# Kernel tuning notes

Measured on AMD Instinct MI355X. Metric: run time of the kernel, lower is better.

The kernel has to match this reference:

```python
import jax, jax.numpy as jnp
import numpy as np

NAF, NBF, DT = 64, 32, 1
B, GROUP = 2000, 100
P = B * GROUP

def _lin(key, din, dout):
    kw, kb = jax.random.split(key)
    return (jax.random.normal(kw, (din, dout), jnp.float32) * 0.02,
            jax.random.normal(kb, (dout,), jnp.float32) * 0.01)

def setup_inputs() -> dict:
    key = jax.random.key(0)
    ks = jax.random.split(key, 12)
    pairs = jax.random.normal(ks[0], (P, 2 * NAF + NBF), jnp.float32)
    idx_pairs = jnp.full((B,), GROUP, dtype=jnp.int32)
    ref_feats = jax.random.normal(ks[1], (B, 32), jnp.float32)
    aw, ab = _lin(ks[2], NAF, 128)
    bw, bb = _lin(ks[3], NBF, 128)
    p1w, p1b = _lin(ks[4], 384, 512)
    p2w, p2b = _lin(ks[5], 512, 256)
    p3w, p3b = _lin(ks[6], 256, 1024)
    f1w, f1b = _lin(ks[7], 1024, 512)
    f2w, f2b = _lin(ks[8], 512, 32)
    f3w, f3b = _lin(ks[9], 32, DT)
    return dict(pairs=pairs, idx_pairs=idx_pairs, ref_feats=ref_feats,
                aw=aw, ab=ab, bw=bw, bb=bb,
                p1w=p1w, p1b=p1b, p2w=p2w, p2b=p2b, p3w=p3w, p3b=p3b,
                f1w=f1w, f1b=f1b, f2w=f2w, f2b=f2b, f3w=f3w, f3b=f3b)

def reference(pairs, idx_pairs, ref_feats,
              aw, ab, bw, bb,
              p1w, p1b, p2w, p2b, p3w, p3b,
              f1w, f1b, f2w, f2b, f3w, f3b):
    relu = jax.nn.relu
    a1 = relu(pairs[:, :NAF] @ aw + ab)            # [P,128]
    a2 = relu(pairs[:, NAF:2 * NAF] @ aw + ab)     # [P,128]
    be = relu(pairs[:, 2 * NAF:] @ bw + bb)        # [P,128]
    h = jnp.concatenate([a1, a2, be], axis=1)      # [P,384]
    h = relu(h @ p1w + p1b)
    h = relu(h @ p2w + p2b)
    x = h @ p3w + p3b                              # [P,1024]
    nb = idx_pairs.shape[0]
    seg = jnp.repeat(jnp.arange(nb, dtype=jnp.int32), idx_pairs,
                     total_repeat_length=x.shape[0])
    sums = jax.ops.segment_sum(x, seg, num_segments=nb)
    h_pair = sums / idx_pairs[:, None].astype(x.dtype)  # segment mean [B,1024]
    h = relu(h_pair @ f1w + f1b)
    h = relu(h @ f2w + f2b)
    return h @ f3w + f3b                           # [B,1]
```

## Files before the change

kernel.cpp:

```cpp
#include <hip/hip_runtime.h>
#include <cstdint>
#include <cstddef>


typedef __bf16 bf16;
typedef __attribute__((ext_vector_type(8))) __bf16 bf16x8;
typedef __attribute__((ext_vector_type(4))) __bf16 bf16x4;
typedef __attribute__((ext_vector_type(4))) float floatx4;

#define GRP 100
#define NWIN 3125

#define WOFF_AW 0
#define WOFF_BW 8192
#define WOFF_P1 12288
#define WOFF_P2 208896
#define WOFF_P3 339968
#define WOFF_F1 602112
#define WOFF_F2 1126400
#define WOFF_HS 1142784
#define WOFF_HP 4342784
#define WOFF_H2 6390784

#define LSTR_P  168
#define LSTR_H  392
#define LSTR_H2 136
#define LSTR_MS 264

static __device__ __forceinline__ floatx4 mfma16(bf16x8 a, bf16x8 b, floatx4 c) {
  return __builtin_amdgcn_mfma_f32_16x16x32_bf16(a, b, c, 0, 0, 0);
}

__global__ __launch_bounds__(256) void pack_lds(
    const float* __restrict__ aw, const float* __restrict__ bw,
    const float* __restrict__ p1w, const float* __restrict__ p2w,
    const float* __restrict__ p3w, const float* __restrict__ f1w,
    const float* __restrict__ f2w, bf16* __restrict__ wpk) {
  __shared__ float t[32][65];
  const int tid = threadIdx.x;
  int b = blockIdx.x;

  if (b < 550) {
    const float* src; int dstoff, K, N, tt;
    if (b < 4)        { src = aw;  dstoff = WOFF_AW; K = 64;   N = 128;  tt = b; }
    else if (b < 6)   { src = bw;  dstoff = WOFF_BW; K = 32;   N = 128;  tt = b - 4; }
    else if (b < 102) { src = p1w; dstoff = WOFF_P1; K = 384;  N = 512;  tt = b - 6; }
    else if (b < 166) { src = p2w; dstoff = WOFF_P2; K = 512;  N = 256;  tt = b - 102; }
    else if (b < 294) { src = p3w; dstoff = WOFF_P3; K = 256;  N = 1024; tt = b - 166; }
    else              { src = f1w; dstoff = WOFF_F1; K = 1024; N = 512;  tt = b - 294; }
    const int KT = K >> 5;
    const int kt = tt % KT;
    const int n0 = (tt / KT) * 64;
    for (int i = tid; i < 2048; i += 256) {
      int r = i >> 6, c = i & 63;
      t[r][c] = src[(size_t)(kt * 32 + r) * N + n0 + c];
    }
    __syncthreads();
    const int nc = n0 >> 7, nl0 = n0 & 127;
    bf16* dst = wpk + dstoff + ((size_t)(nc * KT + kt) * 128 + nl0) * 32;
    int o = tid * 8;
    int nl = o >> 5, kk = o & 31;
    bf16x8 v;
#pragma unroll
    for (int i = 0; i < 8; ++i) v[i] = (bf16)t[kk + i][nl];
    *(bf16x8*)(dst + nl * 32 + kk) = v;
  } else {
    const int kt = b - 550;
    for (int i = tid; i < 1024; i += 256) {
      int r = i >> 5, c = i & 31;
      t[r][c] = f2w[(size_t)(kt * 32 + r) * 32 + c];
    }
    __syncthreads();
    if (tid < 128) {
      int o = tid * 8;
      int nl = o >> 5, kk = o & 31;
      bf16x8 v;
#pragma unroll
      for (int i = 0; i < 8; ++i) v[i] = (bf16)t[kk + i][nl];
      *(bf16x8*)(wpk + WOFF_F2 + kt * 1024 + nl * 32 + kk) = v;
    }
  }
}

static __device__ __forceinline__ void kstep2(const bf16* __restrict__ Ab,
                                              int astride, int acol,
                                              const bf16* __restrict__ b0p,
                                              const bf16* __restrict__ b1p,
                                              floatx4* acc, int lm, int lq) {
  bf16x8 b0 = *(const bf16x8*)b0p;
  bf16x8 b1 = *(const bf16x8*)b1p;
#pragma unroll
  for (int mt = 0; mt < 4; ++mt) {
    bf16x8 a = *(const bf16x8*)(Ab + (mt * 16 + lm) * astride + acol + lq * 8);
    acc[mt * 2]     = mfma16(a, b0, acc[mt * 2]);
    acc[mt * 2 + 1] = mfma16(a, b1, acc[mt * 2 + 1]);
  }
}

static __device__ __forceinline__ void epi2(const floatx4* acc,
                                            const float* __restrict__ bias,
                                            bf16* dst, int dstride, int w,
                                            int lm, int lq) {
#pragma unroll
  for (int mt = 0; mt < 4; ++mt)
#pragma unroll
    for (int j = 0; j < 2; ++j) {
      int col = (w + 4 * j) * 16 + lm;
      float bv = bias[col];
      floatx4 c = acc[mt * 2 + j];
#pragma unroll
      for (int r = 0; r < 4; ++r) {
        float v = c[r] + bv;
        v = v > 0.f ? v : 0.f;
        dst[(mt * 16 + lq * 4 + r) * dstride + col] = (bf16)v;
      }
    }
}

__global__ __launch_bounds__(256, 2) void seg_kernel(
    const float* __restrict__ pairs, const float* __restrict__ ab,
    const float* __restrict__ bb, const float* __restrict__ p1b,
    const float* __restrict__ p2b, const bf16* __restrict__ wpk,
    float* __restrict__ hsum) {
  __shared__ __align__(16) bf16 hbuf[64 * LSTR_H];
  __shared__ __align__(16) bf16 pbuf[64 * LSTR_P];

  const int tid = threadIdx.x;
  const int w = tid >> 6;
  const int lane = tid & 63;
  const int lm = lane & 15;
  const int lq = lane >> 4;
  const int blk = blockIdx.x;

  {
    const float4* src = (const float4*)(pairs + (size_t)blk * (64 * 160));
    for (int i = tid; i < 64 * 40; i += 256) {
      int row = i / 40;
      int c4 = (i - row * 40) * 4;
      float4 v = src[i];
      bf16x4 o = {(bf16)v.x, (bf16)v.y, (bf16)v.z, (bf16)v.w};
      *(bf16x4*)(pbuf + row * LSTR_P + c4) = o;
    }
  }
  __syncthreads();

  const floatx4 fz = {0.f, 0.f, 0.f, 0.f};
  floatx4 acc[8];
  floatx4 acc3[16];

#pragma unroll
  for (int t = 0; t < 8; ++t) acc[t] = fz;
#pragma unroll
  for (int kt = 0; kt < 2; ++kt)
    kstep2(pbuf, LSTR_P, kt * 32,
           wpk + WOFF_AW + ((size_t)(kt * 128 + w * 16 + lm)) * 32 + lq * 8,
           wpk + WOFF_AW + ((size_t)(kt * 128 + (w + 4) * 16 + lm)) * 32 + lq * 8,
           acc, lm, lq);
  epi2(acc, ab, hbuf, LSTR_H, w, lm, lq);
#pragma unroll
  for (int t = 0; t < 8; ++t) acc[t] = fz;
#pragma unroll
  for (int kt = 0; kt < 2; ++kt)
    kstep2(pbuf, LSTR_P, 64 + kt * 32,
           wpk + WOFF_AW + ((size_t)(kt * 128 + w * 16 + lm)) * 32 + lq * 8,
           wpk + WOFF_AW + ((size_t)(kt * 128 + (w + 4) * 16 + lm)) * 32 + lq * 8,
           acc, lm, lq);
  epi2(acc, ab, hbuf + 128, LSTR_H, w, lm, lq);
#pragma unroll
  for (int t = 0; t < 8; ++t) acc[t] = fz;
  kstep2(pbuf, LSTR_P, 128,
         wpk + WOFF_BW + ((size_t)(w * 16 + lm)) * 32 + lq * 8,
         wpk + WOFF_BW + ((size_t)((w + 4) * 16 + lm)) * 32 + lq * 8,
         acc, lm, lq);
  epi2(acc, bb, hbuf + 256, LSTR_H, w, lm, lq);

  __syncthreads();

#pragma unroll
  for (int t = 0; t < 16; ++t) acc3[t] = fz;

  for (int nc = 0; nc < 4; ++nc) {
#pragma unroll
    for (int t = 0; t < 8; ++t) acc[t] = fz;

    {
      const bf16* bp = wpk + WOFF_P1 +
          ((size_t)(nc * 12) * 128 + w * 16 + lm) * 32 + lq * 8;
      bf16x8 b0n = *(const bf16x8*)(bp);
      bf16x8 b1n = *(const bf16x8*)(bp + 2048);
      bf16x8 an[4];
#pragma unroll
      for (int mt = 0; mt < 4; ++mt)
        an[mt] = *(const bf16x8*)(hbuf + (mt * 16 + lm) * LSTR_H + lq * 8);
#pragma unroll
      for (int kt = 0; kt < 12; ++kt) {
        bf16x8 b0 = b0n, b1 = b1n;
        bf16x8 ac[4];
#pragma unroll
        for (int mt = 0; mt < 4; ++mt) ac[mt] = an[mt];
        if (kt < 11) {
          b0n = *(const bf16x8*)(bp + (size_t)(kt + 1) * 4096);
          b1n = *(const bf16x8*)(bp + (size_t)(kt + 1) * 4096 + 2048);
#pragma unroll
          for (int mt = 0; mt < 4; ++mt)
            an[mt] = *(const bf16x8*)(hbuf + (mt * 16 + lm) * LSTR_H +
                                      (kt + 1) * 32 + lq * 8);
        }
        __builtin_amdgcn_s_setprio(1);
#pragma unroll
        for (int mt = 0; mt < 4; ++mt) {
          acc[mt * 2]     = mfma16(ac[mt], b0, acc[mt * 2]);
          acc[mt * 2 + 1] = mfma16(ac[mt], b1, acc[mt * 2 + 1]);
        }
        __builtin_amdgcn_s_setprio(0);
      }
    }
    __syncthreads();
    epi2(acc, p1b + nc * 128, pbuf, LSTR_H2, w, lm, lq);
    __syncthreads();

    {
      const bf16* bp = wpk + WOFF_P2 +
          ((size_t)(((w >> 1) * 16 + nc * 4) * 128 + (w & 1) * 64 + lm)) * 32 +
          lq * 8;
      bf16x8 bn[4];
#pragma unroll
      for (int j = 0; j < 4; ++j) bn[j] = *(const bf16x8*)(bp + j * 512);
      bf16x8 an[4];
#pragma unroll
      for (int mt = 0; mt < 4; ++mt)
        an[mt] = *(const bf16x8*)(pbuf + (mt * 16 + lm) * LSTR_H2 + lq * 8);
#pragma unroll
      for (int kt2 = 0; kt2 < 4; ++kt2) {
        bf16x8 bc[4], ac[4];
#pragma unroll
        for (int j = 0; j < 4; ++j) bc[j] = bn[j];
#pragma unroll
        for (int mt = 0; mt < 4; ++mt) ac[mt] = an[mt];
        if (kt2 < 3) {
#pragma unroll
          for (int j = 0; j < 4; ++j)
            bn[j] = *(const bf16x8*)(bp + (size_t)(kt2 + 1) * 4096 + j * 512);
#pragma unroll
          for (int mt = 0; mt < 4; ++mt)
            an[mt] = *(const bf16x8*)(pbuf + (mt * 16 + lm) * LSTR_H2 +
                                      (kt2 + 1) * 32 + lq * 8);
        }
        __builtin_amdgcn_s_setprio(1);
#pragma unroll
        for (int mt = 0; mt < 4; ++mt)
#pragma unroll
          for (int j = 0; j < 4; ++j)
            acc3[mt * 4 + j] = mfma16(ac[mt], bc[j], acc3[mt * 4 + j]);
        __builtin_amdgcn_s_setprio(0);
      }
    }
  }

  const int s0 = (64 * blk) / 100;
  const int sp = (s0 + 1) * 100 - 64 * blk;
  floatx4 msk[4];
#pragma unroll
  for (int mt = 0; mt < 4; ++mt)
#pragma unroll
    for (int r = 0; r < 4; ++r)
      msk[mt][r] = (mt * 16 + lq * 4 + r < sp) ? 1.f : 0.f;

#pragma unroll
  for (int s = 0; s < 4; ++s) {
    int cl = w * 64 + s * 16 + lm;
    float bv = p2b[cl];
    float tot = 0.f, cs0 = 0.f;
#pragma unroll
    for (int mt = 0; mt < 4; ++mt) {
      floatx4 c = acc3[mt * 4 + s];
#pragma unroll
      for (int r = 0; r < 4; ++r) {
        float v = c[r] + bv;
        v = v > 0.f ? v : 0.f;
        tot += v;
        cs0 = fmaf(v, msk[mt][r], cs0);
      }
    }
    float cs1 = tot - cs0;
    cs0 += __shfl_xor(cs0, 16, 64);
    cs0 += __shfl_xor(cs0, 32, 64);
    cs1 += __shfl_xor(cs1, 16, 64);
    cs1 += __shfl_xor(cs1, 32, 64);
    if (lq == 0) {
      hsum[(size_t)(2 * blk) * 256 + cl]     = cs0;
      hsum[(size_t)(2 * blk + 1) * 256 + cl] = cs1;
    }
  }
}

__global__ __launch_bounds__(256, 2) void mid_kernel(
    const bf16* __restrict__ wpk, const float* __restrict__ hsum,
    const int* __restrict__ idxp, const float* __restrict__ p3b,
    bf16* __restrict__ hpair) {
  __shared__ __align__(16) bf16 ms[16 * LSTR_MS];

  const int tid = threadIdx.x;
  const int w = tid >> 6;
  const int lane = tid & 63;
  const int lm = lane & 15;
  const int lq = lane >> 4;
  const int r0 = blockIdx.x * 16;

  for (int i = tid; i < 16 * 64; i += 256) {
    int row = i >> 6, c4 = i & 63;
    int seg = r0 + row;
    int b_lo = (100 * seg) >> 6;
    int b_hi = (100 * seg + 99) >> 6;
    float4 sa = {0.f, 0.f, 0.f, 0.f};
    for (int b = b_lo; b <= b_hi; ++b) {
      int slot = (64 * b >= 100 * seg) ? 0 : 1;
      float4 v = *(const float4*)(hsum + (size_t)(2 * b + slot) * 256 + c4 * 4);
      sa.x += v.x; sa.y += v.y; sa.z += v.z; sa.w += v.w;
    }
    float inv = 1.f / (float)idxp[seg];
    bf16x4 o = {(bf16)(sa.x * inv), (bf16)(sa.y * inv),
                (bf16)(sa.z * inv), (bf16)(sa.w * inv)};
    *(bf16x4*)(ms + row * LSTR_MS + c4 * 4) = o;
  }
  __syncthreads();

  const floatx4 fz = {0.f, 0.f, 0.f, 0.f};
#pragma unroll
  for (int ncl = 0; ncl < 2; ++ncl) {
    int nc = 2 * w + ncl;
#pragma unroll
    for (int nt2 = 0; nt2 < 4; ++nt2) {
      floatx4 a2[2];
      a2[0] = fz; a2[1] = fz;
#pragma unroll
      for (int kt = 0; kt < 8; ++kt) {
        bf16x8 a = *(const bf16x8*)(ms + lm * LSTR_MS + kt * 32 + lq * 8);
#pragma unroll
        for (int j = 0; j < 2; ++j) {
          bf16x8 b = *(const bf16x8*)(wpk + WOFF_P3 +
              ((size_t)((nc * 8 + kt) * 128 + (nt2 * 2 + j) * 16 + lm)) * 32 +
              lq * 8);
          a2[j] = mfma16(a, b, a2[j]);
        }
      }
#pragma unroll
      for (int j = 0; j < 2; ++j) {
        int col = nc * 128 + (nt2 * 2 + j) * 16 + lm;
        float bv = p3b[col];
#pragma unroll
        for (int r = 0; r < 4; ++r)
          hpair[(size_t)(r0 + lq * 4 + r) * 1024 + col] = (bf16)(a2[j][r] + bv);
      }
    }
  }
}

__global__ __launch_bounds__(256, 2) void head1_kernel(
    const bf16* __restrict__ wpk, const bf16* __restrict__ hpair,
    const float* __restrict__ f1b, bf16* __restrict__ h2) {
  const int tid = threadIdx.x;
  const int w = tid >> 6;
  const int lane = tid & 63;
  const int lm = lane & 15;
  const int lq = lane >> 4;
  const int rg = blockIdx.x >> 2;
  const int cc = blockIdx.x & 3;
  const int r0 = rg * 16;
  const floatx4 fz = {0.f, 0.f, 0.f, 0.f};

  floatx4 a2[2];
  a2[0] = fz; a2[1] = fz;
#pragma unroll 8
  for (int kt = 0; kt < 32; ++kt) {
    bf16x8 a = *(const bf16x8*)(hpair + (size_t)(r0 + lm) * 1024 + kt * 32 + lq * 8);
#pragma unroll
    for (int j = 0; j < 2; ++j) {
      bf16x8 b = *(const bf16x8*)(wpk + WOFF_F1 +
                    ((size_t)((cc * 32 + kt) * 128 + (2 * w + j) * 16 + lm)) * 32 + lq * 8);
      a2[j] = mfma16(a, b, a2[j]);
    }
  }
#pragma unroll
  for (int j = 0; j < 2; ++j) {
    int col = cc * 128 + (2 * w + j) * 16 + lm;
    float bv = f1b[col];
#pragma unroll
    for (int r = 0; r < 4; ++r) {
      float v = a2[j][r] + bv;
      v = v > 0.f ? v : 0.f;
      h2[(size_t)(r0 + lq * 4 + r) * 512 + col] = (bf16)v;
    }
  }
}

__global__ __launch_bounds__(256, 2) void head2_kernel(
    const bf16* __restrict__ wpk, const bf16* __restrict__ h2,
    const float* __restrict__ f2b, const float* __restrict__ f3w,
    const float* __restrict__ f3b, float* __restrict__ out) {
  __shared__ __align__(16) bf16 h3s[4][16 * 40];

  const int tid = threadIdx.x;
  const int w = tid >> 6;
  const int lane = tid & 63;
  const int lm = lane & 15;
  const int lq = lane >> 4;
  const int rg = blockIdx.x * 4 + w;
  if (rg >= 125) return;
  const int r0 = rg * 16;
  const floatx4 fz = {0.f, 0.f, 0.f, 0.f};

  floatx4 c2[2];
  c2[0] = fz; c2[1] = fz;
#pragma unroll
  for (int kt = 0; kt < 16; ++kt) {
    bf16x8 a = *(const bf16x8*)(h2 + (size_t)(r0 + lm) * 512 + kt * 32 + lq * 8);
#pragma unroll
    for (int j = 0; j < 2; ++j) {
      bf16x8 b = *(const bf16x8*)(wpk + WOFF_F2 +
                    ((size_t)(kt * 32 + j * 16 + lm)) * 32 + lq * 8);
      c2[j] = mfma16(a, b, c2[j]);
    }
  }
#pragma unroll
  for (int j = 0; j < 2; ++j) {
    int col = j * 16 + lm;
    float bv = f2b[col];
#pragma unroll
    for (int r = 0; r < 4; ++r) {
      float v = c2[j][r] + bv;
      v = v > 0.f ? v : 0.f;
      h3s[w][(lq * 4 + r) * 40 + col] = (bf16)v;
    }
  }
  float ps = 0.f;
#pragma unroll
  for (int jj = 0; jj < 8; ++jj)
    ps += (float)h3s[w][lm * 40 + lq * 8 + jj] * f3w[lq * 8 + jj];
  ps += __shfl_xor(ps, 16, 64);
  ps += __shfl_xor(ps, 32, 64);
  if (lq == 0) out[r0 + lm] = ps + f3b[0];
}

extern "C" void kernel_launch(void* const* d_in, const int* in_sizes, int n_in,
                              void* d_out, int out_size, void* d_ws,
                              size_t ws_size, hipStream_t stream) {
  (void)in_sizes; (void)n_in; (void)out_size; (void)ws_size;
  const float* pairs = (const float*)d_in[0];
  const int*   idxp  = (const int*)d_in[1];
  const float* aw  = (const float*)d_in[3];
  const float* ab  = (const float*)d_in[4];
  const float* bw  = (const float*)d_in[5];
  const float* bb  = (const float*)d_in[6];
  const float* p1w = (const float*)d_in[7];
  const float* p1b = (const float*)d_in[8];
  const float* p2w = (const float*)d_in[9];
  const float* p2b = (const float*)d_in[10];
  const float* p3w = (const float*)d_in[11];
  const float* p3b = (const float*)d_in[12];
  const float* f1w = (const float*)d_in[13];
  const float* f1b = (const float*)d_in[14];
  const float* f2w = (const float*)d_in[15];
  const float* f2b = (const float*)d_in[16];
  const float* f3w = (const float*)d_in[17];
  const float* f3b = (const float*)d_in[18];

  bf16* wpk = (bf16*)d_ws;
  float* hsum = (float*)(wpk + WOFF_HS);
  bf16* hpair = wpk + WOFF_HP;
  bf16* h2 = wpk + WOFF_H2;

  pack_lds<<<566, 256, 0, stream>>>(aw, bw, p1w, p2w, p3w, f1w, f2w, wpk);
  seg_kernel<<<NWIN, 256, 0, stream>>>(pairs, ab, bb, p1b, p2b, wpk, hsum);
  mid_kernel<<<125, 256, 0, stream>>>(wpk, hsum, idxp, p3b, hpair);
  head1_kernel<<<500, 256, 0, stream>>>(wpk, hpair, f1b, h2);
  head2_kernel<<<32, 256, 0, stream>>>(wpk, h2, f2b, f3w, f3b,
                                       (float*)d_out);
}
```

Before: 436.1 us.

## Fuse mid, head1, head2 into one tail kernel; double-buffer weight prefetch

Merges the three post-segment kernels (p3 projection, f1, f2/f3 head) into a single 512-thread kernel per 16-row group. The intermediate activations now stay in LDS instead of making a round trip through global memory, and two kernel launches go away. Separately, the p1 and p2 weight loads in the segment kernel now prefetch two k-steps ahead instead of one. The trade-off is that the tail runs on only 125 blocks, so the f1 stage has less parallelism than the old 500-block launch, and the deeper prefetch raises register pressure.

```diff
diff --git a/kernel.cpp b/kernel.cpp
--- a/kernel.cpp
+++ b/kernel.cpp
@@ -19,8 +19,6 @@
 #define WOFF_F1 602112
 #define WOFF_F2 1126400
 #define WOFF_HS 1142784
-#define WOFF_HP 4342784
-#define WOFF_H2 6390784
 
 #define LSTR_P  168
 #define LSTR_H  392
@@ -186,25 +184,30 @@
     {
       const bf16* bp = wpk + WOFF_P1 +
           ((size_t)(nc * 12) * 128 + w * 16 + lm) * 32 + lq * 8;
-      bf16x8 b0n = *(const bf16x8*)(bp);
-      bf16x8 b1n = *(const bf16x8*)(bp + 2048);
+      bf16x8 bs0[2], bs1[2];
+      bs0[0] = *(const bf16x8*)(bp);
+      bs1[0] = *(const bf16x8*)(bp + 2048);
+      bs0[1] = *(const bf16x8*)(bp + 4096);
+      bs1[1] = *(const bf16x8*)(bp + 4096 + 2048);
       bf16x8 an[4];
 #pragma unroll
       for (int mt = 0; mt < 4; ++mt)
         an[mt] = *(const bf16x8*)(hbuf + (mt * 16 + lm) * LSTR_H + lq * 8);
 #pragma unroll
       for (int kt = 0; kt < 12; ++kt) {
-        bf16x8 b0 = b0n, b1 = b1n;
+        bf16x8 b0 = bs0[kt & 1], b1 = bs1[kt & 1];
         bf16x8 ac[4];
 #pragma unroll
         for (int mt = 0; mt < 4; ++mt) ac[mt] = an[mt];
         if (kt < 11) {
-          b0n = *(const bf16x8*)(bp + (size_t)(kt + 1) * 4096);
-          b1n = *(const bf16x8*)(bp + (size_t)(kt + 1) * 4096 + 2048);
 #pragma unroll
           for (int mt = 0; mt < 4; ++mt)
             an[mt] = *(const bf16x8*)(hbuf + (mt * 16 + lm) * LSTR_H +
                                       (kt + 1) * 32 + lq * 8);
+        }
+        if (kt < 10) {
+          bs0[kt & 1] = *(const bf16x8*)(bp + (size_t)(kt + 2) * 4096);
+          bs1[kt & 1] = *(const bf16x8*)(bp + (size_t)(kt + 2) * 4096 + 2048);
         }
         __builtin_amdgcn_s_setprio(1);
 #pragma unroll
@@ -223,9 +226,12 @@
       const bf16* bp = wpk + WOFF_P2 +
           ((size_t)(((w >> 1) * 16 + nc * 4) * 128 + (w & 1) * 64 + lm)) * 32 +
           lq * 8;
-      bf16x8 bn[4];
-#pragma unroll
-      for (int j = 0; j < 4; ++j) bn[j] = *(const bf16x8*)(bp + j * 512);
+      bf16x8 bs[2][4];
+#pragma unroll
+      for (int j = 0; j < 4; ++j) {
+        bs[0][j] = *(const bf16x8*)(bp + j * 512);
+        bs[1][j] = *(const bf16x8*)(bp + 4096 + j * 512);
+      }
       bf16x8 an[4];
 #pragma unroll
       for (int mt = 0; mt < 4; ++mt)
@@ -234,17 +240,20 @@
       for (int kt2 = 0; kt2 < 4; ++kt2) {
         bf16x8 bc[4], ac[4];
 #pragma unroll
-        for (int j = 0; j < 4; ++j) bc[j] = bn[j];
+        for (int j = 0; j < 4; ++j) bc[j] = bs[kt2 & 1][j];
 #pragma unroll
         for (int mt = 0; mt < 4; ++mt) ac[mt] = an[mt];
         if (kt2 < 3) {
-#pragma unroll
-          for (int j = 0; j < 4; ++j)
-            bn[j] = *(const bf16x8*)(bp + (size_t)(kt2 + 1) * 4096 + j * 512);
 #pragma unroll
           for (int mt = 0; mt < 4; ++mt)
             an[mt] = *(const bf16x8*)(pbuf + (mt * 16 + lm) * LSTR_H2 +
                                       (kt2 + 1) * 32 + lq * 8);
+        }
+        if (kt2 < 2) {
+#pragma unroll
+          for (int j = 0; j < 4; ++j)
+            bs[kt2 & 1][j] =
+                *(const bf16x8*)(bp + (size_t)(kt2 + 2) * 4096 + j * 512);
         }
         __builtin_amdgcn_s_setprio(1);
 #pragma unroll
@@ -294,11 +303,16 @@
   }
 }
 
-__global__ __launch_bounds__(256, 2) void mid_kernel(
+__global__ __launch_bounds__(512, 2) void tail_kernel(
     const bf16* __restrict__ wpk, const float* __restrict__ hsum,
     const int* __restrict__ idxp, const float* __restrict__ p3b,
-    bf16* __restrict__ hpair) {
+    const float* __restrict__ f1b, const float* __restrict__ f2b,
+    const float* __restrict__ f3w, const float* __restrict__ f3b,
+    float* __restrict__ out) {
   __shared__ __align__(16) bf16 ms[16 * LSTR_MS];
+  __shared__ __align__(16) bf16 hp[16 * 1032];
+  __shared__ __align__(16) bf16 h2s[16 * 520];
+  __shared__ __align__(16) bf16 h3s[16 * 40];
 
   const int tid = threadIdx.x;
   const int w = tid >> 6;
@@ -306,8 +320,9 @@
   const int lm = lane & 15;
   const int lq = lane >> 4;
   const int r0 = blockIdx.x * 16;
-
-  for (int i = tid; i < 16 * 64; i += 256) {
+  const floatx4 fz = {0.f, 0.f, 0.f, 0.f};
+
+  for (int i = tid; i < 16 * 64; i += 512) {
     int row = i >> 6, c4 = i & 63;
     int seg = r0 + row;
     int b_lo = (100 * seg) >> 6;
@@ -325,121 +340,89 @@
   }
   __syncthreads();
 
-  const floatx4 fz = {0.f, 0.f, 0.f, 0.f};
-#pragma unroll
-  for (int ncl = 0; ncl < 2; ++ncl) {
-    int nc = 2 * w + ncl;
-#pragma unroll
-    for (int nt2 = 0; nt2 < 4; ++nt2) {
-      floatx4 a2[2];
-      a2[0] = fz; a2[1] = fz;
-#pragma unroll
-      for (int kt = 0; kt < 8; ++kt) {
-        bf16x8 a = *(const bf16x8*)(ms + lm * LSTR_MS + kt * 32 + lq * 8);
-#pragma unroll
-        for (int j = 0; j < 2; ++j) {
-          bf16x8 b = *(const bf16x8*)(wpk + WOFF_P3 +
-              ((size_t)((nc * 8 + kt) * 128 + (nt2 * 2 + j) * 16 + lm)) * 32 +
-              lq * 8);
-          a2[j] = mfma16(a, b, a2[j]);
-        }
-      }
+#pragma unroll
+  for (int nt2 = 0; nt2 < 4; ++nt2) {
+    floatx4 a2[2];
+    a2[0] = fz; a2[1] = fz;
+#pragma unroll
+    for (int kt = 0; kt < 8; ++kt) {
+      bf16x8 a = *(const bf16x8*)(ms + lm * LSTR_MS + kt * 32 + lq * 8);
 #pragma unroll
       for (int j = 0; j < 2; ++j) {
-        int col = nc * 128 + (nt2 * 2 + j) * 16 + lm;
-        float bv = p3b[col];
-#pragma unroll
-        for (int r = 0; r < 4; ++r)
-          hpair[(size_t)(r0 + lq * 4 + r) * 1024 + col] = (bf16)(a2[j][r] + bv);
-      }
-    }
-  }
-}
-
-__global__ __launch_bounds__(256, 2) void head1_kernel(
-    const bf16* __restrict__ wpk, const bf16* __restrict__ hpair,
-    const float* __restrict__ f1b, bf16* __restrict__ h2) {
-  const int tid = threadIdx.x;
-  const int w = tid >> 6;
-  const int lane = tid & 63;
-  const int lm = lane & 15;
-  const int lq = lane >> 4;
-  const int rg = blockIdx.x >> 2;
-  const int cc = blockIdx.x & 3;
-  const int r0 = rg * 16;
-  const floatx4 fz = {0.f, 0.f, 0.f, 0.f};
-
-  floatx4 a2[2];
-  a2[0] = fz; a2[1] = fz;
+        bf16x8 b = *(const bf16x8*)(wpk + WOFF_P3 +
+            ((size_t)((w * 8 + kt) * 128 + (nt2 * 2 + j) * 16 + lm)) * 32 +
+            lq * 8);
+        a2[j] = mfma16(a, b, a2[j]);
+      }
+    }
+#pragma unroll
+    for (int j = 0; j < 2; ++j) {
+      int col = w * 128 + (nt2 * 2 + j) * 16 + lm;
+      float bv = p3b[col];
+#pragma unroll
+      for (int r = 0; r < 4; ++r)
+        hp[(lq * 4 + r) * 1032 + col] = (bf16)(a2[j][r] + bv);
+    }
+  }
+  __syncthreads();
+
+  {
+    floatx4 a4[4];
+#pragma unroll
+    for (int j = 0; j < 4; ++j) a4[j] = fz;
 #pragma unroll 8
-  for (int kt = 0; kt < 32; ++kt) {
-    bf16x8 a = *(const bf16x8*)(hpair + (size_t)(r0 + lm) * 1024 + kt * 32 + lq * 8);
-#pragma unroll
-    for (int j = 0; j < 2; ++j) {
-      bf16x8 b = *(const bf16x8*)(wpk + WOFF_F1 +
-                    ((size_t)((cc * 32 + kt) * 128 + (2 * w + j) * 16 + lm)) * 32 + lq * 8);
-      a2[j] = mfma16(a, b, a2[j]);
-    }
-  }
-#pragma unroll
-  for (int j = 0; j < 2; ++j) {
-    int col = cc * 128 + (2 * w + j) * 16 + lm;
-    float bv = f1b[col];
+    for (int kt = 0; kt < 32; ++kt) {
+      bf16x8 a = *(const bf16x8*)(hp + lm * 1032 + kt * 32 + lq * 8);
+#pragma unroll
+      for (int j = 0; j < 4; ++j) {
+        bf16x8 b = *(const bf16x8*)(wpk + WOFF_F1 +
+            ((size_t)(((w >> 1) * 32 + kt) * 128 + (w & 1) * 64 + j * 16 + lm)) * 32 +
+            lq * 8);
+        a4[j] = mfma16(a, b, a4[j]);
+      }
+    }
+#pragma unroll
+    for (int j = 0; j < 4; ++j) {
+      int col = w * 64 + j * 16 + lm;
+      float bv = f1b[col];
+#pragma unroll
+      for (int r = 0; r < 4; ++r) {
+        float v = a4[j][r] + bv;
+        v = v > 0.f ? v : 0.f;
+        h2s[(lq * 4 + r) * 520 + col] = (bf16)v;
+      }
+    }
+  }
+  __syncthreads();
+
+  if (w < 2) {
+    floatx4 c2 = fz;
+#pragma unroll
+    for (int kt = 0; kt < 16; ++kt) {
+      bf16x8 a = *(const bf16x8*)(h2s + lm * 520 + kt * 32 + lq * 8);
+      bf16x8 b = *(const bf16x8*)(wpk + WOFF_F2 +
+                    ((size_t)(kt * 32 + w * 16 + lm)) * 32 + lq * 8);
+      c2 = mfma16(a, b, c2);
+    }
+    int col = w * 16 + lm;
+    float bv = f2b[col];
 #pragma unroll
     for (int r = 0; r < 4; ++r) {
-      float v = a2[j][r] + bv;
+      float v = c2[r] + bv;
       v = v > 0.f ? v : 0.f;
-      h2[(size_t)(r0 + lq * 4 + r) * 512 + col] = (bf16)v;
-    }
-  }
-}
-
-__global__ __launch_bounds__(256, 2) void head2_kernel(
-    const bf16* __restrict__ wpk, const bf16* __restrict__ h2,
-    const float* __restrict__ f2b, const float* __restrict__ f3w,
-    const float* __restrict__ f3b, float* __restrict__ out) {
-  __shared__ __align__(16) bf16 h3s[4][16 * 40];
-
-  const int tid = threadIdx.x;
-  const int w = tid >> 6;
-  const int lane = tid & 63;
-  const int lm = lane & 15;
-  const int lq = lane >> 4;
-  const int rg = blockIdx.x * 4 + w;
-  if (rg >= 125) return;
-  const int r0 = rg * 16;
-  const floatx4 fz = {0.f, 0.f, 0.f, 0.f};
-
-  floatx4 c2[2];
-  c2[0] = fz; c2[1] = fz;
-#pragma unroll
-  for (int kt = 0; kt < 16; ++kt) {
-    bf16x8 a = *(const bf16x8*)(h2 + (size_t)(r0 + lm) * 512 + kt * 32 + lq * 8);
-#pragma unroll
-    for (int j = 0; j < 2; ++j) {
-      bf16x8 b = *(const bf16x8*)(wpk + WOFF_F2 +
-                    ((size_t)(kt * 32 + j * 16 + lm)) * 32 + lq * 8);
-      c2[j] = mfma16(a, b, c2[j]);
-    }
-  }
-#pragma unroll
-  for (int j = 0; j < 2; ++j) {
-    int col = j * 16 + lm;
-    float bv = f2b[col];
-#pragma unroll
-    for (int r = 0; r < 4; ++r) {
-      float v = c2[j][r] + bv;
-      v = v > 0.f ? v : 0.f;
-      h3s[w][(lq * 4 + r) * 40 + col] = (bf16)v;
-    }
-  }
-  float ps = 0.f;
-#pragma unroll
-  for (int jj = 0; jj < 8; ++jj)
-    ps += (float)h3s[w][lm * 40 + lq * 8 + jj] * f3w[lq * 8 + jj];
-  ps += __shfl_xor(ps, 16, 64);
-  ps += __shfl_xor(ps, 32, 64);
-  if (lq == 0) out[r0 + lm] = ps + f3b[0];
+      h3s[(lq * 4 + r) * 40 + col] = (bf16)v;
+    }
+  }
+  __syncthreads();
+  if (w == 0) {
+    float ps = 0.f;
+#pragma unroll
+    for (int jj = 0; jj < 8; ++jj)
+      ps += (float)h3s[lm * 40 + lq * 8 + jj] * f3w[lq * 8 + jj];
+    ps += __shfl_xor(ps, 16, 64);
+    ps += __shfl_xor(ps, 32, 64);
+    if (lq == 0) out[r0 + lm] = ps + f3b[0];
+  }
 }
 
 extern "C" void kernel_launch(void* const* d_in, const int* in_sizes, int n_in,
@@ -467,13 +450,9 @@
 
   bf16* wpk = (bf16*)d_ws;
   float* hsum = (float*)(wpk + WOFF_HS);
-  bf16* hpair = wpk + WOFF_HP;
-  bf16* h2 = wpk + WOFF_H2;
 
   pack_lds<<<566, 256, 0, stream>>>(aw, bw, p1w, p2w, p3w, f1w, f2w, wpk);
   seg_kernel<<<NWIN, 256, 0, stream>>>(pairs, ab, bb, p1b, p2b, wpk, hsum);
-  mid_kernel<<<125, 256, 0, stream>>>(wpk, hsum, idxp, p3b, hpair);
-  head1_kernel<<<500, 256, 0, stream>>>(wpk, hpair, f1b, h2);
-  head2_kernel<<<32, 256, 0, stream>>>(wpk, h2, f2b, f3w, f3b,
-                                       (float*)d_out);
-}
+  tail_kernel<<<125, 512, 0, stream>>>(wpk, hsum, idxp, p3b, f1b, f2b, f3w,
+                                       f3b, (float*)d_out);
+}
```

Result: faster. 415.3 us (-4.8%).
